# Performance work log

Hardware: AMD Instinct MI355X
Metric: run time of the kernel (lower is better)

Reference implementation:

```python
import jax, jax.numpy as jnp
import numpy as np

N_MOD = 2      # len(l_matrix)
N_SUB = 4096   # each l_matrix entry
DIM = 64
K = 20
ALPHA = 3.0
N = N_MOD * N_SUB  # 8192 total nodes


def setup_inputs() -> dict:
    key = jax.random.key(0)
    k1, k2, k3, k4 = jax.random.split(key, 4)
    nmat = N_MOD * N_MOD
    emb1 = 0.1 * jax.random.normal(k1, (nmat, N_SUB, DIM), dtype=jnp.float32)
    emb2 = 0.1 * jax.random.normal(k2, (nmat, N_SUB, DIM), dtype=jnp.float32)
    # __init__ sets w1/w2 to identity, b to zeros; perturb slightly so they matter
    eye = jnp.eye(DIM, dtype=jnp.float32)
    w1 = eye[None] + 0.01 * jax.random.normal(k3, (nmat, DIM, DIM), dtype=jnp.float32)
    w2 = eye[None] + 0.01 * jax.random.normal(k4, (nmat, DIM, DIM), dtype=jnp.float32)
    b1 = jnp.zeros((nmat, DIM), dtype=jnp.float32)
    b2 = jnp.zeros((nmat, DIM), dtype=jnp.float32)
    idx = jnp.arange(N, dtype=jnp.int64) if jax.config.jax_enable_x64 else jnp.arange(N, dtype=jnp.int32)
    return {"idx": idx, "emb1": emb1, "emb2": emb2, "w1": w1, "w2": w2, "b1": b1, "b2": b2}


def reference(idx, emb1, emb2, w1, w2, b1, b2):
    # per-block linear: nodevec = emb @ w + b   (batched over the nmatrix blocks)
    v1 = jnp.einsum('knd,kde->kne', emb1, w1) + b1[:, None, :]   # [nmat, N_SUB, DIM]
    v2 = jnp.einsum('kmd,kde->kme', emb2, w2) + b2[:, None, :]
    # per-block score: relu(tanh(alpha * v1 @ v2^T))
    a = jnp.einsum('kne,kme->knm', v1, v2)                       # [nmat, N_SUB, N_SUB]
    blocks = jax.nn.relu(jnp.tanh(ALPHA * a))
    # assemble full adjacency: block (i,j) at index i*n_mod + j
    adj = blocks.reshape(N_MOD, N_MOD, N_SUB, N_SUB)
    adj = adj.transpose(0, 2, 1, 3).reshape(N, N)                # [N, N]
    # row-wise topk mask (mask=1 at topk positions), adj * mask
    vals, cols = jax.lax.top_k(adj, K)                           # [N, K]
    rows = jnp.arange(N)[:, None]
    out = jnp.zeros_like(adj).at[rows, cols].set(vals)
    return out


if __name__ == "__main__":
    out = reference(**setup_inputs())
    print(out.shape, float(out.sum()))
```

## Files before the change

### kernel.cpp

```cpp
#include <hip/hip_runtime.h>
#include <hip/hip_bf16.h>

#define NSUB 4096
#define DIM 64
#define NROW 8192
#define KTOP 20
#define CAND 64

typedef unsigned long long u64;
typedef __attribute__((ext_vector_type(8))) short bf16x8;
typedef __attribute__((ext_vector_type(4))) float f32x4;

__device__ __forceinline__ unsigned umax(unsigned a, unsigned b) { return a > b ? a : b; }
__device__ __forceinline__ unsigned umin(unsigned a, unsigned b) { return a < b ? a : b; }

__global__ __launch_bounds__(256) void k_compute_v(
        const float* __restrict__ emb1, const float* __restrict__ w1,
        const float* __restrict__ b1,
        const float* __restrict__ emb2, const float* __restrict__ w2,
        const float* __restrict__ b2,
        double* __restrict__ V1d, double* __restrict__ V2d,
        unsigned short* __restrict__ V1b, unsigned short* __restrict__ V2b) {
    __shared__ alignas(16) float embS[64 * 64];
    __shared__ alignas(16) float wS[64 * 64];
    __shared__ float bS[64];

    int bx    = blockIdx.x;
    int which = bx >> 8;
    int rem   = bx & 255;
    int k     = rem >> 6;
    int tile  = rem & 63;
    int n0    = tile * 64;

    const float* emb = which ? emb2 : emb1;
    const float* w   = which ? w2 : w1;
    const float* b   = which ? b2 : b1;
    double* Vd = which ? V2d : V1d;
    unsigned short* Vb = which ? V2b : V1b;

    int tid = threadIdx.x;
    const float* esrc = emb + ((size_t)k * NSUB + n0) * DIM;
    const float* wsrc = w + (size_t)k * DIM * DIM;
    for (int t = tid; t < 64 * 64; t += 256) { embS[t] = esrc[t]; wS[t] = wsrc[t]; }
    if (tid < 64) bS[tid] = b[k * 64 + tid];
    __syncthreads();

    int e    = tid & 63;
    int mrow = tid >> 6;

    double accs[16];
#pragma unroll
    for (int it = 0; it < 16; ++it) accs[it] = (double)bS[e];

    for (int dg = 0; dg < 16; ++dg) {
        double wv[4];
#pragma unroll
        for (int q = 0; q < 4; ++q) wv[q] = (double)wS[(dg * 4 + q) * 64 + e];
#pragma unroll
        for (int it = 0; it < 16; ++it) {
            float4 em = *(const float4*)&embS[(mrow * 16 + it) * 64 + dg * 4];
            accs[it] += (double)em.x * wv[0] + (double)em.y * wv[1]
                      + (double)em.z * wv[2] + (double)em.w * wv[3];
        }
    }

#pragma unroll
    for (int it = 0; it < 16; ++it) {
        size_t o = ((size_t)k * NSUB + n0 + mrow * 16 + it) * DIM + e;
        Vd[o] = accs[it];
        __hip_bfloat16 hv = __float2bfloat16((float)accs[it]);
        Vb[o] = *reinterpret_cast<unsigned short*>(&hv);
    }
}

__global__ __launch_bounds__(256) void k_stage1(const unsigned short* __restrict__ V1b,
                                                const unsigned short* __restrict__ V2b,
                                                unsigned int* __restrict__ S1) {
    int tid = threadIdx.x;
    int l = tid & 63;
    int w = tid >> 6;
    int bx = blockIdx.x;
    int rt = bx >> 2;
    int h  = (bx >> 1) & 1;
    int q2 = bx & 1;
    int r0 = rt * 64;
    int i  = r0 >> 12;
    int n0 = r0 & (NSUB - 1);
    int kb = 2 * i + h;
    int q  = l >> 4;

    bf16x8 a0[4], a1[4];
#pragma unroll
    for (int t = 0; t < 4; ++t) {
        const unsigned short* ap =
            V1b + ((size_t)kb * NSUB + n0 + t * 16 + (l & 15)) * DIM + (q * 8);
        a0[t] = *(const bf16x8*)ap;
        a1[t] = *(const bf16x8*)(ap + 32);
    }

    int coff = q2 * 2048 + w * 512;
    const unsigned short* bp =
        V2b + ((size_t)kb * NSUB + coff + (l & 15)) * DIM + (q * 8);

    float m1[16], m2[16];
#pragma unroll
    for (int sl = 0; sl < 16; ++sl) { m1[sl] = 0.f; m2[sl] = 0.f; }

    bf16x8 cb0 = *(const bf16x8*)bp;
    bf16x8 cb1 = *(const bf16x8*)(bp + 32);
    bp += 16 * DIM;

    for (int s = 0; s < 32; ++s) {
        bf16x8 nb0, nb1;
        if (s < 31) {
            nb0 = *(const bf16x8*)bp;
            nb1 = *(const bf16x8*)(bp + 32);
            bp += 16 * DIM;
        }
#pragma unroll
        for (int t = 0; t < 4; ++t) {
            f32x4 acc = {0.f, 0.f, 0.f, 0.f};
            acc = __builtin_amdgcn_mfma_f32_16x16x32_bf16(a0[t], cb0, acc, 0, 0, 0);
            acc = __builtin_amdgcn_mfma_f32_16x16x32_bf16(a1[t], cb1, acc, 0, 0, 0);
#pragma unroll
            for (int r = 0; r < 4; ++r) {
                int sl = t * 4 + r;
                float v = acc[r];
                m2[sl] = __builtin_amdgcn_fmed3f(v, m1[sl], m2[sl]);
                m1[sl] = fmaxf(m1[sl], v);
            }
        }
        if ((s & 15) == 15) {
#pragma unroll
            for (int st = 1; st <= 8; st <<= 1) {
#pragma unroll
                for (int sl = 0; sl < 16; ++sl) {
                    float o1 = __shfl_xor(m1[sl], st);
                    float o2 = __shfl_xor(m2[sl], st);
                    float nm1 = fmaxf(m1[sl], o1);
                    float nm2 = fmaxf(fminf(m1[sl], o1), fmaxf(m2[sl], o2));
                    m1[sl] = nm1; m2[sl] = nm2;
                }
            }
            if ((l & 15) == 0) {
                int gblk = h * 16 + q2 * 8 + w * 2 + (s >> 4);
#pragma unroll
                for (int sl = 0; sl < 16; ++sl) {
                    int rowg = r0 + (sl >> 2) * 16 + q * 4 + (sl & 3);
                    uint2 vv;
                    vv.x = __float_as_uint(m1[sl]);
                    vv.y = __float_as_uint(m2[sl]);
                    *(uint2*)&S1[(size_t)rowg * 64 + gblk * 2] = vv;
                }
            }
#pragma unroll
            for (int sl = 0; sl < 16; ++sl) { m1[sl] = 0.f; m2[sl] = 0.f; }
        }
        cb0 = nb0; cb1 = nb1;
    }
}

__global__ __launch_bounds__(256) void k_filter(const unsigned short* __restrict__ V1b,
                                                const unsigned short* __restrict__ V2b,
                                                const unsigned int* __restrict__ S1,
                                                unsigned int* __restrict__ cnt,
                                                int* __restrict__ colsG) {
    __shared__ float Lsh[64];
    int tid = threadIdx.x;
    int l = tid & 63;
    int w = tid >> 6;
    int bx = blockIdx.x;
    int rt = bx >> 2;
    int h  = (bx >> 1) & 1;
    int q2 = bx & 1;
    int r0 = rt * 64;
    int i  = r0 >> 12;
    int n0 = r0 & (NSUB - 1);
    int kb = 2 * i + h;
    int q  = l >> 4;

    for (int rr = 0; rr < 16; ++rr) {
        int rowg = r0 + w * 16 + rr;
        unsigned key = S1[(size_t)rowg * 64 + l];
#pragma unroll
        for (int k = 2; k <= 64; k <<= 1) {
#pragma unroll
            for (int j = k >> 1; j > 0; j >>= 1) {
                unsigned other = (unsigned)__shfl_xor((int)key, j);
                int ixj = l ^ j;
                bool up = ((l & k) == 0);
                bool keepMax = ((l > ixj) == up);
                key = keepMax ? umax(key, other) : umin(key, other);
            }
        }
        if (l == 44) Lsh[w * 16 + rr] = fmaxf(__uint_as_float(key) - 0.006f, 1e-30f);
    }
    __syncthreads();

    bf16x8 a0[4], a1[4];
#pragma unroll
    for (int t = 0; t < 4; ++t) {
        const unsigned short* ap =
            V1b + ((size_t)kb * NSUB + n0 + t * 16 + (l & 15)) * DIM + (q * 8);
        a0[t] = *(const bf16x8*)ap;
        a1[t] = *(const bf16x8*)(ap + 32);
    }

    float Lr[16];
#pragma unroll
    for (int sl = 0; sl < 16; ++sl)
        Lr[sl] = Lsh[(sl >> 2) * 16 + q * 4 + (sl & 3)];

    int coff = q2 * 2048 + w * 512;
    const unsigned short* bp =
        V2b + ((size_t)kb * NSUB + coff + (l & 15)) * DIM + (q * 8);

    bf16x8 cb0 = *(const bf16x8*)bp;
    bf16x8 cb1 = *(const bf16x8*)(bp + 32);
    bp += 16 * DIM;

    for (int s = 0; s < 32; ++s) {
        bf16x8 nb0, nb1;
        if (s < 31) {
            nb0 = *(const bf16x8*)bp;
            nb1 = *(const bf16x8*)(bp + 32);
            bp += 16 * DIM;
        }
        int c = h * 4096 + coff + s * 16 + (l & 15);
#pragma unroll
        for (int t = 0; t < 4; ++t) {
            f32x4 acc = {0.f, 0.f, 0.f, 0.f};
            acc = __builtin_amdgcn_mfma_f32_16x16x32_bf16(a0[t], cb0, acc, 0, 0, 0);
            acc = __builtin_amdgcn_mfma_f32_16x16x32_bf16(a1[t], cb1, acc, 0, 0, 0);
#pragma unroll
            for (int r = 0; r < 4; ++r) {
                int sl = t * 4 + r;
                if (acc[r] >= Lr[sl]) {
                    int rowg = r0 + t * 16 + q * 4 + r;
                    unsigned pos = atomicAdd(&cnt[rowg], 1u);
                    if (pos < CAND) colsG[(size_t)rowg * CAND + pos] = c;
                }
            }
        }
        cb0 = nb0; cb1 = nb1;
    }
}

__global__ __launch_bounds__(256) void k_refine(const double* __restrict__ V1d,
                                                const double* __restrict__ V2d,
                                                const unsigned int* __restrict__ cnt,
                                                const int* __restrict__ colsG,
                                                int* __restrict__ outIdx,
                                                float* __restrict__ outVal) {
    int tid = threadIdx.x;
    int l = tid & 63, w = tid >> 6;
    int row = blockIdx.x * 4 + w;
    int i = row >> 12, n = row & (NSUB - 1);

    unsigned cn = cnt[row];
    if (cn > CAND) cn = CAND;
    bool valid = (unsigned)l < cn;
    int c = valid ? colsG[(size_t)row * CAND + l] : 0;
    int k = 2 * i + (c >> 12);
    int m = c & (NSUB - 1);

    const double* v1p = V1d + ((size_t)k * NSUB + n) * DIM;
    const double* v2p = V2d + ((size_t)k * NSUB + m) * DIM;
    double a = 0.0;
    for (int d = 0; d < DIM; ++d) a += v1p[d] * v2p[d];

    double av = a > 0.0 ? a : 0.0;
    u64 key = (((u64)__double_as_longlong(av)) & ~0x1FFFull) | (u64)(8191 - c);
    if (!valid) key = 0;

    int rank = 0;
    for (int jj = 0; jj < 64; ++jj) {
        u64 kj = (u64)__shfl((long long)key, jj);
        rank += (kj > key || (kj == key && jj < l)) ? 1 : 0;
    }
    if (valid && rank < KTOP) {
        float val = (av > 0.0) ? (float)tanh(3.0 * av) : 0.0f;
        outIdx[(size_t)row * KTOP + rank] = c;
        outVal[(size_t)row * KTOP + rank] = val;
    }
}

__global__ __launch_bounds__(256) void k_write(const int* __restrict__ outIdx,
                                               const float* __restrict__ outVal,
                                               float* __restrict__ out) {
    int t = threadIdx.x;
    size_t base = (size_t)blockIdx.x * 4 * NROW;
    float4 z = {0.f, 0.f, 0.f, 0.f};
    float4* o4 = (float4*)(out + base);
#pragma unroll
    for (int it = 0; it < 32; ++it) o4[it * 256 + t] = z;
    __syncthreads();
    if (t < 4 * KTOP) {
        int row = blockIdx.x * 4 + t / KTOP;
        int c = outIdx[(size_t)blockIdx.x * 4 * KTOP + t];
        float v = outVal[(size_t)blockIdx.x * 4 * KTOP + t];
        out[(size_t)row * NROW + c] = v;
    }
}

extern "C" void kernel_launch(void* const* d_in, const int* in_sizes, int n_in,
                              void* d_out, int out_size, void* d_ws, size_t ws_size,
                              hipStream_t stream) {
    const float* emb1 = (const float*)d_in[1];
    const float* emb2 = (const float*)d_in[2];
    const float* w1   = (const float*)d_in[3];
    const float* w2   = (const float*)d_in[4];
    const float* b1   = (const float*)d_in[5];
    const float* b2   = (const float*)d_in[6];
    float* out = (float*)d_out;

    char* p = (char*)d_out;
    double*         V1d   = (double*)p;
    double*         V2d   = (double*)(p + (size_t)8 * 1024 * 1024);
    unsigned short* V1b   = (unsigned short*)(p + (size_t)16 * 1024 * 1024);
    unsigned short* V2b   = (unsigned short*)(p + (size_t)18 * 1024 * 1024);
    unsigned int*   S1    = (unsigned int*)(p + (size_t)20 * 1024 * 1024);
    int*            colsG = (int*)(p + (size_t)22 * 1024 * 1024);

    int*          outIdx = (int*)d_ws;
    float*        outVal = (float*)((char*)d_ws + (size_t)NROW * KTOP * sizeof(int));
    unsigned int* cntp   = (unsigned int*)((char*)d_ws + (size_t)2 * NROW * KTOP * sizeof(int));

    hipLaunchKernelGGL(k_compute_v, dim3(512), dim3(256), 0, stream,
                       emb1, w1, b1, emb2, w2, b2, V1d, V2d, V1b, V2b);
    hipMemsetAsync(cntp, 0, (size_t)NROW * sizeof(unsigned int), stream);
    hipLaunchKernelGGL(k_stage1, dim3(512), dim3(256), 0, stream, V1b, V2b, S1);
    hipLaunchKernelGGL(k_filter, dim3(512), dim3(256), 0, stream, V1b, V2b, S1, cntp, colsG);
    hipLaunchKernelGGL(k_refine, dim3(2048), dim3(256), 0, stream,
                       V1d, V2d, cntp, colsG, outIdx, outVal);
    hipLaunchKernelGGL(k_write, dim3(2048), dim3(256), 0, stream,
                       outIdx, outVal, out);
}
```

Measured before the change: 448.7 us.

## Fuse refine into filter via last-block atomic, double grid, fold memset

Doubles the grid of the stage1 and filter kernels to 1024 blocks by giving each block a quarter of the columns instead of half. This raises parallelism and occupancy, and launch bounds are added to match. The separate refine kernel is removed: the last of the eight filter blocks covering a row tile, found with an atomic counter and threadfences, runs the fp64 refine and rank step for that tile. The counter memset moves into k_compute_v, which removes two launches, but the refine now runs on only 128 blocks and may serialize at the tail.

```diff
diff --git a/kernel.cpp b/kernel.cpp
--- a/kernel.cpp
+++ b/kernel.cpp
@@ -20,12 +20,18 @@
         const float* __restrict__ emb2, const float* __restrict__ w2,
         const float* __restrict__ b2,
         double* __restrict__ V1d, double* __restrict__ V2d,
-        unsigned short* __restrict__ V1b, unsigned short* __restrict__ V2b) {
+        unsigned short* __restrict__ V1b, unsigned short* __restrict__ V2b,
+        unsigned int* __restrict__ cnt, unsigned int* __restrict__ done) {
     __shared__ alignas(16) float embS[64 * 64];
     __shared__ alignas(16) float wS[64 * 64];
     __shared__ float bS[64];
 
     int bx    = blockIdx.x;
+    int tid   = threadIdx.x;
+
+    if (bx < 32) cnt[bx * 256 + tid] = 0u;
+    if (bx == 32 && tid < 128) done[tid] = 0u;
+
     int which = bx >> 8;
     int rem   = bx & 255;
     int k     = rem >> 6;
@@ -38,7 +44,6 @@
     double* Vd = which ? V2d : V1d;
     unsigned short* Vb = which ? V2b : V1b;
 
-    int tid = threadIdx.x;
     const float* esrc = emb + ((size_t)k * NSUB + n0) * DIM;
     const float* wsrc = w + (size_t)k * DIM * DIM;
     for (int t = tid; t < 64 * 64; t += 256) { embS[t] = esrc[t]; wS[t] = wsrc[t]; }
@@ -73,16 +78,16 @@
     }
 }
 
-__global__ __launch_bounds__(256) void k_stage1(const unsigned short* __restrict__ V1b,
-                                                const unsigned short* __restrict__ V2b,
-                                                unsigned int* __restrict__ S1) {
+__global__ __launch_bounds__(256, 4) void k_stage1(const unsigned short* __restrict__ V1b,
+                                                   const unsigned short* __restrict__ V2b,
+                                                   unsigned int* __restrict__ S1) {
     int tid = threadIdx.x;
     int l = tid & 63;
     int w = tid >> 6;
     int bx = blockIdx.x;
-    int rt = bx >> 2;
-    int h  = (bx >> 1) & 1;
-    int q2 = bx & 1;
+    int rt = bx >> 3;
+    int h  = (bx >> 2) & 1;
+    int e8 = bx & 3;
     int r0 = rt * 64;
     int i  = r0 >> 12;
     int n0 = r0 & (NSUB - 1);
@@ -98,7 +103,7 @@
         a1[t] = *(const bf16x8*)(ap + 32);
     }
 
-    int coff = q2 * 2048 + w * 512;
+    int coff = e8 * 1024 + w * 256;
     const unsigned short* bp =
         V2b + ((size_t)kb * NSUB + coff + (l & 15)) * DIM + (q * 8);
 
@@ -110,9 +115,9 @@
     bf16x8 cb1 = *(const bf16x8*)(bp + 32);
     bp += 16 * DIM;
 
-    for (int s = 0; s < 32; ++s) {
+    for (int s = 0; s < 16; ++s) {
         bf16x8 nb0, nb1;
-        if (s < 31) {
+        if (s < 15) {
             nb0 = *(const bf16x8*)bp;
             nb1 = *(const bf16x8*)(bp + 32);
             bp += 16 * DIM;
@@ -130,49 +135,52 @@
                 m1[sl] = fmaxf(m1[sl], v);
             }
         }
-        if ((s & 15) == 15) {
-#pragma unroll
-            for (int st = 1; st <= 8; st <<= 1) {
-#pragma unroll
-                for (int sl = 0; sl < 16; ++sl) {
-                    float o1 = __shfl_xor(m1[sl], st);
-                    float o2 = __shfl_xor(m2[sl], st);
-                    float nm1 = fmaxf(m1[sl], o1);
-                    float nm2 = fmaxf(fminf(m1[sl], o1), fmaxf(m2[sl], o2));
-                    m1[sl] = nm1; m2[sl] = nm2;
-                }
-            }
-            if ((l & 15) == 0) {
-                int gblk = h * 16 + q2 * 8 + w * 2 + (s >> 4);
-#pragma unroll
-                for (int sl = 0; sl < 16; ++sl) {
-                    int rowg = r0 + (sl >> 2) * 16 + q * 4 + (sl & 3);
-                    uint2 vv;
-                    vv.x = __float_as_uint(m1[sl]);
-                    vv.y = __float_as_uint(m2[sl]);
-                    *(uint2*)&S1[(size_t)rowg * 64 + gblk * 2] = vv;
-                }
-            }
-#pragma unroll
-            for (int sl = 0; sl < 16; ++sl) { m1[sl] = 0.f; m2[sl] = 0.f; }
-        }
         cb0 = nb0; cb1 = nb1;
     }
-}
-
-__global__ __launch_bounds__(256) void k_filter(const unsigned short* __restrict__ V1b,
-                                                const unsigned short* __restrict__ V2b,
-                                                const unsigned int* __restrict__ S1,
-                                                unsigned int* __restrict__ cnt,
-                                                int* __restrict__ colsG) {
+
+#pragma unroll
+    for (int st = 1; st <= 8; st <<= 1) {
+#pragma unroll
+        for (int sl = 0; sl < 16; ++sl) {
+            float o1 = __shfl_xor(m1[sl], st);
+            float o2 = __shfl_xor(m2[sl], st);
+            float nm1 = fmaxf(m1[sl], o1);
+            float nm2 = fmaxf(fminf(m1[sl], o1), fmaxf(m2[sl], o2));
+            m1[sl] = nm1; m2[sl] = nm2;
+        }
+    }
+    if ((l & 15) == 0) {
+        int gblk = h * 16 + e8 * 4 + w;
+#pragma unroll
+        for (int sl = 0; sl < 16; ++sl) {
+            int rowg = r0 + (sl >> 2) * 16 + q * 4 + (sl & 3);
+            uint2 vv;
+            vv.x = __float_as_uint(m1[sl]);
+            vv.y = __float_as_uint(m2[sl]);
+            *(uint2*)&S1[(size_t)rowg * 64 + gblk * 2] = vv;
+        }
+    }
+}
+
+__global__ __launch_bounds__(256, 4) void k_filter(const unsigned short* __restrict__ V1b,
+                                                   const unsigned short* __restrict__ V2b,
+                                                   const unsigned int* __restrict__ S1,
+                                                   unsigned int* __restrict__ cnt,
+                                                   int* __restrict__ colsG,
+                                                   const double* __restrict__ V1d,
+                                                   const double* __restrict__ V2d,
+                                                   unsigned int* __restrict__ done,
+                                                   int* __restrict__ outIdx,
+                                                   float* __restrict__ outVal) {
     __shared__ float Lsh[64];
+    __shared__ int lastS;
     int tid = threadIdx.x;
     int l = tid & 63;
     int w = tid >> 6;
     int bx = blockIdx.x;
-    int rt = bx >> 2;
-    int h  = (bx >> 1) & 1;
-    int q2 = bx & 1;
+    int rt = bx >> 3;
+    int h  = (bx >> 2) & 1;
+    int e8 = bx & 3;
     int r0 = rt * 64;
     int i  = r0 >> 12;
     int n0 = r0 & (NSUB - 1);
@@ -211,7 +219,7 @@
     for (int sl = 0; sl < 16; ++sl)
         Lr[sl] = Lsh[(sl >> 2) * 16 + q * 4 + (sl & 3)];
 
-    int coff = q2 * 2048 + w * 512;
+    int coff = e8 * 1024 + w * 256;
     const unsigned short* bp =
         V2b + ((size_t)kb * NSUB + coff + (l & 15)) * DIM + (q * 8);
 
@@ -219,9 +227,9 @@
     bf16x8 cb1 = *(const bf16x8*)(bp + 32);
     bp += 16 * DIM;
 
-    for (int s = 0; s < 32; ++s) {
+    for (int s = 0; s < 16; ++s) {
         bf16x8 nb0, nb1;
-        if (s < 31) {
+        if (s < 15) {
             nb0 = *(const bf16x8*)bp;
             nb1 = *(const bf16x8*)(bp + 32);
             bp += 16 * DIM;
@@ -244,44 +252,44 @@
         }
         cb0 = nb0; cb1 = nb1;
     }
-}
-
-__global__ __launch_bounds__(256) void k_refine(const double* __restrict__ V1d,
-                                                const double* __restrict__ V2d,
-                                                const unsigned int* __restrict__ cnt,
-                                                const int* __restrict__ colsG,
-                                                int* __restrict__ outIdx,
-                                                float* __restrict__ outVal) {
-    int tid = threadIdx.x;
-    int l = tid & 63, w = tid >> 6;
-    int row = blockIdx.x * 4 + w;
-    int i = row >> 12, n = row & (NSUB - 1);
-
-    unsigned cn = cnt[row];
-    if (cn > CAND) cn = CAND;
-    bool valid = (unsigned)l < cn;
-    int c = valid ? colsG[(size_t)row * CAND + l] : 0;
-    int k = 2 * i + (c >> 12);
-    int m = c & (NSUB - 1);
-
-    const double* v1p = V1d + ((size_t)k * NSUB + n) * DIM;
-    const double* v2p = V2d + ((size_t)k * NSUB + m) * DIM;
-    double a = 0.0;
-    for (int d = 0; d < DIM; ++d) a += v1p[d] * v2p[d];
-
-    double av = a > 0.0 ? a : 0.0;
-    u64 key = (((u64)__double_as_longlong(av)) & ~0x1FFFull) | (u64)(8191 - c);
-    if (!valid) key = 0;
-
-    int rank = 0;
-    for (int jj = 0; jj < 64; ++jj) {
-        u64 kj = (u64)__shfl((long long)key, jj);
-        rank += (kj > key || (kj == key && jj < l)) ? 1 : 0;
-    }
-    if (valid && rank < KTOP) {
-        float val = (av > 0.0) ? (float)tanh(3.0 * av) : 0.0f;
-        outIdx[(size_t)row * KTOP + rank] = c;
-        outVal[(size_t)row * KTOP + rank] = val;
+
+    __threadfence();
+    __syncthreads();
+    if (tid == 0) lastS = (atomicAdd(&done[rt], 1u) == 7u) ? 1 : 0;
+    __syncthreads();
+    if (!lastS) return;
+    __threadfence();
+
+    for (int rr = 0; rr < 16; ++rr) {
+        int row = r0 + w * 16 + rr;
+        int n = row & (NSUB - 1);
+
+        unsigned cn = cnt[row];
+        if (cn > CAND) cn = CAND;
+        bool valid = (unsigned)l < cn;
+        int c = valid ? colsG[(size_t)row * CAND + l] : 0;
+        int kk2 = 2 * i + (c >> 12);
+        int m = c & (NSUB - 1);
+
+        const double* v1p = V1d + ((size_t)kk2 * NSUB + n) * DIM;
+        const double* v2p = V2d + ((size_t)kk2 * NSUB + m) * DIM;
+        double a = 0.0;
+        for (int d = 0; d < DIM; ++d) a += v1p[d] * v2p[d];
+
+        double av = a > 0.0 ? a : 0.0;
+        u64 key = (((u64)__double_as_longlong(av)) & ~0x1FFFull) | (u64)(8191 - c);
+        if (!valid) key = 0;
+
+        int rank = 0;
+        for (int jj = 0; jj < 64; ++jj) {
+            u64 kj = (u64)__shfl((long long)key, jj);
+            rank += (kj > key || (kj == key && jj < l)) ? 1 : 0;
+        }
+        if (valid && rank < KTOP) {
+            float val = (av > 0.0) ? (float)tanh(3.0 * av) : 0.0f;
+            outIdx[(size_t)row * KTOP + rank] = c;
+            outVal[(size_t)row * KTOP + rank] = val;
+        }
     }
 }
 
@@ -325,14 +333,13 @@
     int*          outIdx = (int*)d_ws;
     float*        outVal = (float*)((char*)d_ws + (size_t)NROW * KTOP * sizeof(int));
     unsigned int* cntp   = (unsigned int*)((char*)d_ws + (size_t)2 * NROW * KTOP * sizeof(int));
+    unsigned int* donep  = cntp + NROW;
 
     hipLaunchKernelGGL(k_compute_v, dim3(512), dim3(256), 0, stream,
-                       emb1, w1, b1, emb2, w2, b2, V1d, V2d, V1b, V2b);
-    hipMemsetAsync(cntp, 0, (size_t)NROW * sizeof(unsigned int), stream);
-    hipLaunchKernelGGL(k_stage1, dim3(512), dim3(256), 0, stream, V1b, V2b, S1);
-    hipLaunchKernelGGL(k_filter, dim3(512), dim3(256), 0, stream, V1b, V2b, S1, cntp, colsG);
-    hipLaunchKernelGGL(k_refine, dim3(2048), dim3(256), 0, stream,
-                       V1d, V2d, cntp, colsG, outIdx, outVal);
+                       emb1, w1, b1, emb2, w2, b2, V1d, V2d, V1b, V2b, cntp, donep);
+    hipLaunchKernelGGL(k_stage1, dim3(1024), dim3(256), 0, stream, V1b, V2b, S1);
+    hipLaunchKernelGGL(k_filter, dim3(1024), dim3(256), 0, stream,
+                       V1b, V2b, S1, cntp, colsG, V1d, V2d, donep, outIdx, outVal);
     hipLaunchKernelGGL(k_write, dim3(2048), dim3(256), 0, stream,
                        outIdx, outVal, out);
 }
```

Result: slower. 671.8 us (+49.7%).
